# Kernel tuning notes

Hardware: AMD Instinct MI355X
Metric: run time of the kernel (lower is better)

The kernel has to match this reference:

```python
import jax, jax.numpy as jnp
import numpy as np

MAX_REL_POS = 16


def relative_position_ids(t, max_pos):
    r = jnp.arange(t)
    dist = jnp.clip(r[None, :] - r[:, None], -max_pos, max_pos)
    return dist + max_pos  # [T, T] in [0, 2*max_pos]


def setup_inputs():
    key = jax.random.key(0)
    ks = jax.random.split(key, 5)
    B, H, T, D = 2, 16, 1024, 64
    V = 2 * MAX_REL_POS + 1  # 33
    q = jax.random.normal(ks[0], (B, H, T, D), dtype=jnp.float32)
    k = jax.random.normal(ks[1], (B, H, T, D), dtype=jnp.float32)
    v = jax.random.normal(ks[2], (B, H, T, D), dtype=jnp.float32)
    embed_k = jax.random.normal(ks[3], (V, D), dtype=jnp.float32)
    embed_v = jax.random.normal(ks[4], (V, D), dtype=jnp.float32)
    mask = jnp.zeros((1, 1, T, T), dtype=jnp.float32)
    return {"q": q, "k": k, "v": v, "embed_k": embed_k, "embed_v": embed_v, "mask": mask}


def reference(q, k, v, embed_k, embed_v, mask):
    T = q.shape[2]
    D = k.shape[-1]
    rel = relative_position_ids(T, MAX_REL_POS)           # [T, T] int
    rel_k = embed_k[rel]                                   # [T, T, D]
    rel_v = embed_v[rel]                                   # [T, T, D]
    # QK^T plus relative-key term (matmul_with_relative_representations, transpose_b=True)
    logits = jnp.einsum('bhqd,bhkd->bhqk', q, k) + jnp.einsum('bhqd,qkd->bhqk', q, rel_k)
    logits = logits * (1.0 / jnp.sqrt(jnp.asarray(D, dtype=logits.dtype)))
    logits = logits + mask * (-1e9)
    attn = jax.nn.softmax(logits, axis=-1)                 # [B, H, T, T]
    out = jnp.einsum('bhqk,bhkd->bhqd', attn, v) + jnp.einsum('bhqk,qkd->bhqd', attn, rel_v)
    return out, attn
```

## Files before the change

### kernel.cpp

```cpp
#include <hip/hip_runtime.h>

#define BHN 32
#define T 1024
#define DD 64
#define TQ 16
#define PST 1032

typedef __attribute__((ext_vector_type(8))) __bf16 bf16x8;
typedef __attribute__((ext_vector_type(8))) unsigned short us8;
typedef __attribute__((ext_vector_type(4))) float f32x4;

struct alignas(16) U4 { unsigned a, b, c, d; };

__device__ __forceinline__ unsigned short f2bf(float x) {
  unsigned u = __builtin_bit_cast(unsigned, x);
  u += 0x7fffu + ((u >> 16) & 1u);
  return (unsigned short)(u >> 16);
}
__device__ __forceinline__ float bf2f(unsigned short h) {
  unsigned u = ((unsigned)h) << 16;
  return __builtin_bit_cast(float, u);
}
__device__ __forceinline__ bf16x8 ld_bf16x8(const unsigned short* p) {
  U4 u = *(const U4*)p;
  return __builtin_bit_cast(bf16x8, u);
}

__global__ __launch_bounds__(256) void prep_conv(
    const float* __restrict__ k, const float* __restrict__ v,
    unsigned short* __restrict__ kbf, unsigned short* __restrict__ vt)
{
  __shared__ float sT[64][65];
  const int bh = blockIdx.y;
  const int tb = blockIdx.x * 64;
  const int t = threadIdx.x;
  const size_t base = (size_t)bh * T * DD + (size_t)tb * DD;

  const float4* ksrc = (const float4*)(k + base);
  ushort4* kdst = (ushort4*)(kbf + base);
#pragma unroll
  for (int i = 0; i < 4; ++i) {
    int g = i * 256 + t;
    float4 f = ksrc[g];
    ushort4 u;
    u.x = f2bf(f.x); u.y = f2bf(f.y); u.z = f2bf(f.z); u.w = f2bf(f.w);
    kdst[g] = u;
  }

  const float* vsrc = v + base;
#pragma unroll
  for (int i = 0; i < 16; ++i) {
    int e = i * 256 + t;
    sT[e & 63][e >> 6] = vsrc[e];
  }
  __syncthreads();
  unsigned short* vdst = vt + (size_t)bh * DD * T + tb;
#pragma unroll
  for (int i = 0; i < 16; ++i) {
    int e = i * 256 + t;
    int dd = e >> 6, kk = e & 63;
    vdst[(size_t)dd * T + kk] = f2bf(sT[dd][kk]);
  }
}

__global__ __launch_bounds__(256, 4) void attn_main(
    const float* __restrict__ q, const unsigned short* __restrict__ kbf,
    const unsigned short* __restrict__ vt, const float* __restrict__ ek,
    const float* __restrict__ ev, const float* __restrict__ mask,
    float* __restrict__ out, float* __restrict__ attn)
{
  __shared__ unsigned short sP[TQ * PST];
  __shared__ float sQek[TQ][33];
  __shared__ float sDiag[TQ][31];
  __shared__ float sRS[4][TQ];
  __shared__ float sRB[4][TQ];
  __shared__ float sInv[TQ];
  __shared__ float sB0n[TQ];

  const int bh = blockIdx.y;
  const int qb = blockIdx.x * TQ;
  const int tid = threadIdx.x;
  const int wave = tid >> 6;
  const int lane = tid & 63;
  const int quad = lane >> 4;
  const int col = lane & 15;

  for (int i = tid; i < TQ * 31; i += 256) (&sDiag[0][0])[i] = 0.f;

  const float* qrows = q + (size_t)bh * T * DD + (size_t)qb * DD;
  for (int idx = tid; idx < TQ * 33; idx += 256) {
    int i = idx / 33;
    int r = idx - i * 33;
    const float4* qa = (const float4*)(qrows + i * DD);
    const float4* eb = (const float4*)(ek + r * DD);
    float acc = 0.f;
#pragma unroll
    for (int d4 = 0; d4 < 16; ++d4) {
      float4 a = qa[d4], b = eb[d4];
      acc += a.x * b.x + a.y * b.y + a.z * b.z + a.w * b.w;
    }
    sQek[i][r] = acc;
  }
  __syncthreads();

  bf16x8 aq0, aq1;
  {
    const float* qp = qrows + col * DD + quad * 8;
    float4 f0 = *(const float4*)(qp);
    float4 f1 = *(const float4*)(qp + 4);
    float4 f2 = *(const float4*)(qp + 32);
    float4 f3 = *(const float4*)(qp + 36);
    us8 u0, u1;
    u0[0] = f2bf(f0.x); u0[1] = f2bf(f0.y); u0[2] = f2bf(f0.z); u0[3] = f2bf(f0.w);
    u0[4] = f2bf(f1.x); u0[5] = f2bf(f1.y); u0[6] = f2bf(f1.z); u0[7] = f2bf(f1.w);
    u1[0] = f2bf(f2.x); u1[1] = f2bf(f2.y); u1[2] = f2bf(f2.z); u1[3] = f2bf(f2.w);
    u1[4] = f2bf(f3.x); u1[5] = f2bf(f3.y); u1[6] = f2bf(f3.z); u1[7] = f2bf(f3.w);
    aq0 = __builtin_bit_cast(bf16x8, u0);
    aq1 = __builtin_bit_cast(bf16x8, u1);
  }

  float regS[4] = {0.f, 0.f, 0.f, 0.f};
  float regB[4] = {0.f, 0.f, 0.f, 0.f};
  const unsigned short* kbh = kbf + (size_t)bh * T * DD;
  for (int it = 0; it < 16; ++it) {
    int kt = wave * 256 + it * 16;
    const unsigned short* kp = kbh + (size_t)(kt + col) * DD + quad * 8;
    bf16x8 bk0 = ld_bf16x8(kp);
    bf16x8 bk1 = ld_bf16x8(kp + 32);
    f32x4 acc = {0.f, 0.f, 0.f, 0.f};
    acc = __builtin_amdgcn_mfma_f32_16x16x32_bf16(aq0, bk0, acc, 0, 0, 0);
    acc = __builtin_amdgcn_mfma_f32_16x16x32_bf16(aq1, bk1, acc, 0, 0, 0);
    int kg = kt + col;
#pragma unroll
    for (int r = 0; r < 4; ++r) {
      int row = quad * 4 + r;
      int qg = qb + row;
      int dk = kg - qg;
      int rel = dk < -16 ? 0 : (dk > 16 ? 32 : dk + 16);
      float logit = (acc[r] + sQek[row][rel]) * 0.125f
                  + mask[(size_t)qg * T + kg] * (-1e9f);
      float p = __expf(fminf(logit, 80.f));
      sP[row * PST + kg] = f2bf(p);
      regS[r] += p;
      if (dk <= -16) regB[r] += p;
      if ((unsigned)(dk + 15) < 31u) sDiag[row][dk + 15] = p;
    }
  }

#pragma unroll
  for (int r = 0; r < 4; ++r) {
    float s = regS[r], b = regB[r];
#pragma unroll
    for (int off = 1; off < 16; off <<= 1) {
      s += __shfl_xor(s, off, 64);
      b += __shfl_xor(b, off, 64);
    }
    if (col == 0) { sRS[wave][quad * 4 + r] = s; sRB[wave][quad * 4 + r] = b; }
  }
  __syncthreads();
  if (tid < TQ) {
    float S = sRS[0][tid] + sRS[1][tid] + sRS[2][tid] + sRS[3][tid];
    float B0 = sRB[0][tid] + sRB[1][tid] + sRB[2][tid] + sRB[3][tid];
    float inv = 1.f / S;
    sInv[tid] = inv;
    sB0n[tid] = B0 * inv;
  }
  __syncthreads();

  float* attnq = attn + (size_t)bh * T * T + (size_t)qb * T;
#pragma unroll
  for (int i = 0; i < 16; ++i) {
    int e = i * 256 + tid;
    int row = e >> 8;
    int c4 = (e & 255) * 4;
    float inv = sInv[row];
    const unsigned short* pp = &sP[row * PST + c4];
    float4 o;
    o.x = bf2f(pp[0]) * inv;
    o.y = bf2f(pp[1]) * inv;
    o.z = bf2f(pp[2]) * inv;
    o.w = bf2f(pp[3]) * inv;
    *(float4*)(attnq + (size_t)row * T + c4) = o;
  }

  const unsigned short* vtw = vt + (size_t)bh * DD * T + (size_t)(wave * 16 + col) * T;
  f32x4 oacc = {0.f, 0.f, 0.f, 0.f};
  for (int kc = 0; kc < 32; ++kc) {
    bf16x8 ap = ld_bf16x8(&sP[col * PST + kc * 32 + quad * 8]);
    bf16x8 bv = ld_bf16x8(vtw + kc * 32 + quad * 8);
    oacc = __builtin_amdgcn_mfma_f32_16x16x32_bf16(ap, bv, oacc, 0, 0, 0);
  }

  const int dcol = wave * 16 + col;
  float ev0 = ev[dcol];
  float ev32 = ev[32 * DD + dcol];
  float invr[4], accv[4];
#pragma unroll
  for (int r = 0; r < 4; ++r) {
    int row = quad * 4 + r;
    float inv = sInv[row];
    invr[r] = inv;
    float sumd = 0.f;
#pragma unroll
    for (int j = 0; j < 31; ++j) sumd += sDiag[row][j];
    float b0 = sB0n[row];
    float b32 = 1.f - b0 - sumd * inv;
    accv[r] = oacc[r] * inv + b0 * ev0 + b32 * ev32;
  }
  for (int j = 0; j < 31; ++j) {
    float e = ev[(j + 1) * DD + dcol];
#pragma unroll
    for (int r = 0; r < 4; ++r)
      accv[r] += sDiag[quad * 4 + r][j] * invr[r] * e;
  }
  float* outp = out + (size_t)bh * T * DD + (size_t)qb * DD;
#pragma unroll
  for (int r = 0; r < 4; ++r)
    outp[(size_t)(quad * 4 + r) * DD + dcol] = accv[r];
}

extern "C" void kernel_launch(void* const* d_in, const int* in_sizes, int n_in,
                              void* d_out, int out_size, void* d_ws, size_t ws_size,
                              hipStream_t stream) {
  const float* q    = (const float*)d_in[0];
  const float* k    = (const float*)d_in[1];
  const float* v    = (const float*)d_in[2];
  const float* ek   = (const float*)d_in[3];
  const float* ev   = (const float*)d_in[4];
  const float* mask = (const float*)d_in[5];

  float* out  = (float*)d_out;
  float* attn = out + (size_t)BHN * T * DD;

  unsigned short* kbf = (unsigned short*)d_ws;
  unsigned short* vt  = kbf + (size_t)BHN * T * DD;

  dim3 pg(T / 64, BHN);
  prep_conv<<<pg, 256, 0, stream>>>(k, v, kbf, vt);

  dim3 g(T / TQ, BHN);
  attn_main<<<g, 256, 0, stream>>>(q, kbf, vt, ek, ev, mask, out, attn);
}
```

Baseline: 276.8 us.

## Recompute QK logits in second pass instead of staging full P tile in LDS

Removes the 33KB bf16 probability buffer from shared memory. Pass one now only accumulates row sums, and a second pass recomputes QK^T and the exponentials, writes normalized attention directly with nontemporal stores, and feeds a small per-wave tile into the PV MFMA. Each wave handles its own key range across all 64 output columns, and the partial outputs are reduced through LDS. Launch bounds rise to 6 blocks per CU, trading doubled QK and exp work plus extra K loads for higher occupancy and less LDS traffic.

```diff
diff --git a/kernel.cpp b/kernel.cpp
--- a/kernel.cpp
+++ b/kernel.cpp
@@ -4,7 +4,6 @@
 #define T 1024
 #define DD 64
 #define TQ 16
-#define PST 1032
 
 typedef __attribute__((ext_vector_type(8))) __bf16 bf16x8;
 typedef __attribute__((ext_vector_type(8))) unsigned short us8;
@@ -63,19 +62,20 @@
   }
 }
 
-__global__ __launch_bounds__(256, 4) void attn_main(
+__global__ __launch_bounds__(256, 6) void attn_main(
     const float* __restrict__ q, const unsigned short* __restrict__ kbf,
     const unsigned short* __restrict__ vt, const float* __restrict__ ek,
     const float* __restrict__ ev, const float* __restrict__ mask,
     float* __restrict__ out, float* __restrict__ attn)
 {
-  __shared__ unsigned short sP[TQ * PST];
   __shared__ float sQek[TQ][33];
   __shared__ float sDiag[TQ][31];
   __shared__ float sRS[4][TQ];
   __shared__ float sRB[4][TQ];
   __shared__ float sInv[TQ];
   __shared__ float sB0n[TQ];
+  __shared__ alignas(16) unsigned short sTile[4][16][40];
+  __shared__ float sOr[4][TQ][66];
 
   const int bh = blockIdx.y;
   const int qb = blockIdx.x * TQ;
@@ -124,13 +124,13 @@
   const unsigned short* kbh = kbf + (size_t)bh * T * DD;
   for (int it = 0; it < 16; ++it) {
     int kt = wave * 256 + it * 16;
-    const unsigned short* kp = kbh + (size_t)(kt + col) * DD + quad * 8;
+    int kg = kt + col;
+    const unsigned short* kp = kbh + (size_t)kg * DD + quad * 8;
     bf16x8 bk0 = ld_bf16x8(kp);
     bf16x8 bk1 = ld_bf16x8(kp + 32);
     f32x4 acc = {0.f, 0.f, 0.f, 0.f};
     acc = __builtin_amdgcn_mfma_f32_16x16x32_bf16(aq0, bk0, acc, 0, 0, 0);
     acc = __builtin_amdgcn_mfma_f32_16x16x32_bf16(aq1, bk1, acc, 0, 0, 0);
-    int kg = kt + col;
 #pragma unroll
     for (int r = 0; r < 4; ++r) {
       int row = quad * 4 + r;
@@ -140,7 +140,6 @@
       float logit = (acc[r] + sQek[row][rel]) * 0.125f
                   + mask[(size_t)qg * T + kg] * (-1e9f);
       float p = __expf(fminf(logit, 80.f));
-      sP[row * PST + kg] = f2bf(p);
       regS[r] += p;
       if (dk <= -16) regB[r] += p;
       if ((unsigned)(dk + 15) < 31u) sDiag[row][dk + 15] = p;
@@ -167,56 +166,85 @@
   }
   __syncthreads();
 
+  float invr[4];
+#pragma unroll
+  for (int r = 0; r < 4; ++r) invr[r] = sInv[quad * 4 + r];
+
   float* attnq = attn + (size_t)bh * T * T + (size_t)qb * T;
-#pragma unroll
-  for (int i = 0; i < 16; ++i) {
-    int e = i * 256 + tid;
-    int row = e >> 8;
-    int c4 = (e & 255) * 4;
+  const unsigned short* vtb = vt + (size_t)bh * DD * T;
+  f32x4 zero4 = {0.f, 0.f, 0.f, 0.f};
+  f32x4 oacc[4];
+#pragma unroll
+  for (int dt = 0; dt < 4; ++dt) oacc[dt] = zero4;
+
+  for (int c = 0; c < 8; ++c) {
+#pragma unroll
+    for (int sub = 0; sub < 2; ++sub) {
+      const int it = c * 2 + sub;
+      const int kt = wave * 256 + it * 16;
+      const int kg = kt + col;
+      const unsigned short* kp = kbh + (size_t)kg * DD + quad * 8;
+      bf16x8 bk0 = ld_bf16x8(kp);
+      bf16x8 bk1 = ld_bf16x8(kp + 32);
+      f32x4 acc = {0.f, 0.f, 0.f, 0.f};
+      acc = __builtin_amdgcn_mfma_f32_16x16x32_bf16(aq0, bk0, acc, 0, 0, 0);
+      acc = __builtin_amdgcn_mfma_f32_16x16x32_bf16(aq1, bk1, acc, 0, 0, 0);
+#pragma unroll
+      for (int r = 0; r < 4; ++r) {
+        int row = quad * 4 + r;
+        int qg = qb + row;
+        int dk = kg - qg;
+        int rel = dk < -16 ? 0 : (dk > 16 ? 32 : dk + 16);
+        float logit = (acc[r] + sQek[row][rel]) * 0.125f
+                    + mask[(size_t)qg * T + kg] * (-1e9f);
+        float p = __expf(fminf(logit, 80.f));
+        __builtin_nontemporal_store(p * invr[r], attnq + (size_t)row * T + kg);
+        sTile[wave][row][sub * 16 + col] = f2bf(p);
+      }
+    }
+    bf16x8 ap = ld_bf16x8(&sTile[wave][col][quad * 8]);
+    const unsigned short* vp = vtb + (size_t)col * T + (wave * 256 + c * 32 + quad * 8);
+#pragma unroll
+    for (int dt = 0; dt < 4; ++dt) {
+      bf16x8 bv = ld_bf16x8(vp + (size_t)(dt * 16) * T);
+      oacc[dt] = __builtin_amdgcn_mfma_f32_16x16x32_bf16(ap, bv, oacc[dt], 0, 0, 0);
+    }
+  }
+
+#pragma unroll
+  for (int dt = 0; dt < 4; ++dt)
+#pragma unroll
+    for (int r = 0; r < 4; ++r)
+      sOr[wave][quad * 4 + r][dt * 16 + col] = oacc[dt][r];
+  __syncthreads();
+
+  const int d = tid & 63;
+  float ev0 = ev[d];
+  float ev32 = ev[32 * DD + d];
+  float accv[4], invq[4], sd[4];
+#pragma unroll
+  for (int r = 0; r < 4; ++r) {
+    int row = wave * 4 + r;
+    float o = sOr[0][row][d] + sOr[1][row][d] + sOr[2][row][d] + sOr[3][row][d];
     float inv = sInv[row];
-    const unsigned short* pp = &sP[row * PST + c4];
-    float4 o;
-    o.x = bf2f(pp[0]) * inv;
-    o.y = bf2f(pp[1]) * inv;
-    o.z = bf2f(pp[2]) * inv;
-    o.w = bf2f(pp[3]) * inv;
-    *(float4*)(attnq + (size_t)row * T + c4) = o;
-  }
-
-  const unsigned short* vtw = vt + (size_t)bh * DD * T + (size_t)(wave * 16 + col) * T;
-  f32x4 oacc = {0.f, 0.f, 0.f, 0.f};
-  for (int kc = 0; kc < 32; ++kc) {
-    bf16x8 ap = ld_bf16x8(&sP[col * PST + kc * 32 + quad * 8]);
-    bf16x8 bv = ld_bf16x8(vtw + kc * 32 + quad * 8);
-    oacc = __builtin_amdgcn_mfma_f32_16x16x32_bf16(ap, bv, oacc, 0, 0, 0);
-  }
-
-  const int dcol = wave * 16 + col;
-  float ev0 = ev[dcol];
-  float ev32 = ev[32 * DD + dcol];
-  float invr[4], accv[4];
-#pragma unroll
-  for (int r = 0; r < 4; ++r) {
-    int row = quad * 4 + r;
-    float inv = sInv[row];
-    invr[r] = inv;
-    float sumd = 0.f;
-#pragma unroll
-    for (int j = 0; j < 31; ++j) sumd += sDiag[row][j];
+    invq[r] = inv;
     float b0 = sB0n[row];
-    float b32 = 1.f - b0 - sumd * inv;
-    accv[r] = oacc[r] * inv + b0 * ev0 + b32 * ev32;
+    accv[r] = o * inv + b0 * ev0 + (1.f - b0) * ev32;
+    sd[r] = 0.f;
   }
   for (int j = 0; j < 31; ++j) {
-    float e = ev[(j + 1) * DD + dcol];
-#pragma unroll
-    for (int r = 0; r < 4; ++r)
-      accv[r] += sDiag[quad * 4 + r][j] * invr[r] * e;
+    float e = ev[(j + 1) * DD + d];
+#pragma unroll
+    for (int r = 0; r < 4; ++r) {
+      float pd = sDiag[wave * 4 + r][j];
+      sd[r] += pd;
+      accv[r] += pd * invq[r] * e;
+    }
   }
   float* outp = out + (size_t)bh * T * DD + (size_t)qb * DD;
 #pragma unroll
   for (int r = 0; r < 4; ++r)
-    outp[(size_t)(quad * 4 + r) * DD + dcol] = accv[r];
+    outp[(size_t)(wave * 4 + r) * DD + d] = accv[r] - sd[r] * invq[r] * ev32;
 }
 
 extern "C" void kernel_launch(void* const* d_in, const int* in_sizes, int n_in,
```

New measurement: 314.5 us. 13.6% more time.
